# Kernel tuning notes

Hardware: AMD Instinct MI355X
Metric: run time of the kernel (lower is better)

The kernel has to match this reference:

```python
import jax, jax.numpy as jnp
import numpy as np

B, T, C, H = 4, 4096, 256, 64

def setup_inputs() -> dict:
    key = jax.random.key(0)
    k1, k2, k3, k4 = jax.random.split(key, 4)
    x = jax.random.normal(k1, (B, T, C), dtype=jnp.float32)
    # DenseSynapse weights ~ uniform(-0.1, 0.1); randn spec approximated faithfully in math, init dist irrelevant to correctness
    Wk = jax.random.uniform(k2, (C, H), minval=-0.1, maxval=0.1, dtype=jnp.float32)
    Wq = jax.random.uniform(k3, (C, H), minval=-0.1, maxval=0.1, dtype=jnp.float32)
    Wv = jax.random.uniform(k4, (C, H), minval=-0.1, maxval=0.1, dtype=jnp.float32)
    return {"x": x, "Wk": Wk, "Wq": Wq, "Wv": Wv}

def reference(x, Wk, Wq, Wv):
    Bq, Tq, Cq = x.shape
    # linear projections (DenseSynapse.advance_state with Rscale=1, no bias): x @ W
    k = jnp.einsum('btc,ch->bth', x, Wk)
    q = jnp.einsum('btc,ch->bth', x, Wq)
    v = jnp.einsum('btc,ch->bth', x, Wv)
    # scores scaled by C**-0.5 (n_embd, as in source)
    wei = jnp.einsum('bqh,bkh->bqk', q, k) * (Cq ** -0.5)
    mask = jnp.tril(jnp.ones((Tq, Tq), dtype=bool))
    wei = jnp.where(mask, wei, -jnp.inf)
    wei = jax.nn.softmax(wei, axis=-1)
    # dropout deterministic (eval) in reference
    out = jnp.einsum('bqk,bkh->bqh', wei, v)
    return out
```

## Files before the change

kernel.cpp:

```cpp
#include <hip/hip_runtime.h>
#include <hip/hip_bf16.h>
#include <math.h>

#define Bb   4
#define T    4096
#define Cc   256
#define Hh   64
#define BT   (Bb*T)
#define CHUNK 8
#define CPB  288

using f32x4  = __attribute__((ext_vector_type(4))) float;
using short8 = __attribute__((ext_vector_type(8))) short;

__device__ __forceinline__ ushort f2bf(float f) {
    unsigned u = __builtin_bit_cast(unsigned, f);
    return (ushort)((u + 0x8000u) >> 16);
}
__device__ __forceinline__ float bf2f(ushort u) {
    return __builtin_bit_cast(float, (unsigned)u << 16);
}
__device__ __forceinline__ int swzb(int row, int cb) { return (row<<7) + (cb ^ ((row&7)<<4)); }
__device__ __forceinline__ int swzx(int row, int cb) { return (row<<9) + (cb ^ ((row&7)<<4)); }
__device__ __forceinline__ int chunk_prefix(int qt) {
    const int a = qt >> 3, r = qt & 7;
    return 4*a*(a+1) + r*(a+1);
}

#define GLOAD16(g, l) __builtin_amdgcn_global_load_lds( \
    (const __attribute__((address_space(1))) unsigned*)(g), \
    (__attribute__((address_space(3))) unsigned*)(l), 16, 0, 0)

__global__ __launch_bounds__(256) void wtrans(
    const float* __restrict__ Wq, const float* __restrict__ Wk,
    const float* __restrict__ Wv, ushort* __restrict__ WtG)
{
    __shared__ float wl[256][65];
    const int t = threadIdx.x;
    const int m = blockIdx.x;
    const float* W = (m==0) ? Wq : (m==1) ? Wk : Wv;
    const float scale = (m==0) ? 0.0625f : 1.0f;
    for (int idx = t; idx < 4096; idx += 256) {
        const float4 v4 = ((const float4*)W)[idx];
        const int c = idx >> 4;
        const int h = (idx & 15) * 4;
        wl[c][h+0]=v4.x*scale; wl[c][h+1]=v4.y*scale;
        wl[c][h+2]=v4.z*scale; wl[c][h+3]=v4.w*scale;
    }
    __syncthreads();
    const int h  = t & 63;
    const int n  = m*64 + h;
    const int c0 = (t >> 6) * 64;
    for (int c = c0; c < c0 + 64; c += 4) {
        ushort4 o;
        o.x=f2bf(wl[c+0][h]); o.y=f2bf(wl[c+1][h]);
        o.z=f2bf(wl[c+2][h]); o.w=f2bf(wl[c+3][h]);
        *(ushort4*)((char*)WtG + n*512 + ((c*2) ^ ((n&7)<<4))) = o;
    }
}

__global__ __launch_bounds__(256) void proj_mfma(
    const float* __restrict__ x, const ushort* __restrict__ WtG,
    ushort* __restrict__ qo, ushort* __restrict__ ko, ushort* __restrict__ vtG)
{
    __shared__ ushort xls[64*256];
    __shared__ ushort wls[192*256];
    const int t = threadIdx.x, w = t>>6, lane = t&63, g = lane>>4, ln = lane&15;
    const int blk = blockIdx.x;
    const long rowbase = (long)blk * 64;
    const int b    = blk >> 6;
    const int trow = (blk & 63) * 64;

    {
        const char* src = (const char*)WtG + (long)lane*16;
        for (int c = w; c < 96; c += 4)
            GLOAD16(src + c*1024, (char*)wls + c*1024);
    }
    for (int j = 0; j < 16; ++j) {
        const int idx = t + j*256;
        const int row = idx >> 6;
        const int c4  = (idx & 63) * 4;
        const float4 xv = ((const float4*)x)[(rowbase + row)*64 + (c4>>2)];
        ushort4 o; o.x=f2bf(xv.x); o.y=f2bf(xv.y); o.z=f2bf(xv.z); o.w=f2bf(xv.w);
        *(ushort4*)((char*)xls + swzx(row, c4*2)) = o;
    }
    __syncthreads();

    short8 xf[8];
    #pragma unroll
    for (int ks = 0; ks < 8; ++ks)
        xf[ks] = *(const short8*)((const char*)xls + swzx(w*16+ln, ks*64 + g*16));

    #pragma unroll
    for (int nt = 0; nt < 12; ++nt) {
        f32x4 acc = (f32x4){0.f,0.f,0.f,0.f};
        #pragma unroll
        for (int ks = 0; ks < 8; ++ks) {
            const short8 wf = *(const short8*)((const char*)wls + swzx(nt*16+ln, ks*64 + g*16));
            acc = (nt < 8) ? __builtin_amdgcn_mfma_f32_16x16x32_bf16(wf, xf[ks], acc, 0,0,0)
                           : __builtin_amdgcn_mfma_f32_16x16x32_bf16(xf[ks], wf, acc, 0,0,0);
        }
        ushort4 o; o.x=f2bf(acc[0]); o.y=f2bf(acc[1]); o.z=f2bf(acc[2]); o.w=f2bf(acc[3]);
        if (nt < 4) {
            *(ushort4*)(qo + (rowbase + w*16 + ln)*64 + nt*16 + g*4) = o;
        } else if (nt < 8) {
            *(ushort4*)(ko + (rowbase + w*16 + ln)*64 + (nt-4)*16 + g*4) = o;
        } else {
            *(ushort4*)(vtG + ((long)b*64 + (nt-8)*16 + ln)*T + trow + w*16 + g*4) = o;
        }
    }
}

__global__ __launch_bounds__(256) void attn_mfma(
    const ushort* __restrict__ q, const ushort* __restrict__ k,
    const ushort* __restrict__ vt,
    ushort* __restrict__ part_o, float* __restrict__ part_ml)
{
    __shared__ ushort kls[2][64*64];
    __shared__ ushort vtls[2][64*64];
    __shared__ ushort pls[4][16*64];

    const int bid   = blockIdx.x;
    const int b     = bid & 3;
    const int w2    = (CPB - 1) - (bid >> 2);
    int qt = 0, c = 0;
    {
        int acc = 0;
        for (int qq = 0; qq < 64; ++qq) {
            const int n = (qq >> 3) + 1;
            if (w2 < acc + n) { qt = qq; c = w2 - acc; break; }
            acc += n;
        }
    }
    const int kt0   = c * CHUNK;
    const int ntile = min(qt, kt0 + CHUNK - 1) - kt0 + 1;
    const int pid   = b*CPB + chunk_prefix(qt) + c;

    const int t = threadIdx.x, w = t>>6, lane = t&63, g = lane>>4, ln = lane&15;
    const int lrow = lane >> 3;
    const int lc16 = ((lane & 7) ^ lrow) * 16;
    const char* kbase = (const char*)k  + ((long)b*T)*128;
    const char* vbase = (const char*)vt + ((long)b*64)*(long)T*2;

    #define STAGE(bufi, ktile) do { \
        _Pragma("unroll") for (int j = 0; j < 2; ++j) { const int ci = w*2 + j; \
            GLOAD16(kbase + (long)(ktile)*8192 + ci*1024 + lrow*128 + lc16, \
                    (char*)kls[bufi] + ci*1024); \
            GLOAD16(vbase + ((long)(8*ci + lrow))*8192 + (long)(ktile)*128 + lc16, \
                    (char*)vtls[bufi] + ci*1024); \
        } } while(0)

    short8 qf[2];
    {
        const ushort* qp = q + ((long)(b*T + qt*64 + w*16 + ln))*64;
        qf[0] = *(const short8*)(qp + g*8);
        qf[1] = *(const short8*)(qp + 32 + g*8);
    }
    f32x4 oacc[4];
    #pragma unroll
    for (int i = 0; i < 4; ++i) oacc[i] = (f32x4){0.f,0.f,0.f,0.f};
    float mrun[4], lpart[4];
    #pragma unroll
    for (int r = 0; r < 4; ++r) { mrun[r] = -INFINITY; lpart[r] = 0.f; }

    STAGE(0, kt0);
    for (int it = 0; it < ntile; ++it) {
        const int kt  = kt0 + it;
        const int cur = it & 1;
        __syncthreads();
        if (it + 1 < ntile) STAGE(cur^1, kt + 1);

        f32x4 sf[4];
        #pragma unroll
        for (int i = 0; i < 4; ++i) sf[i] = (f32x4){0.f,0.f,0.f,0.f};
        __builtin_amdgcn_s_setprio(1);
        #pragma unroll
        for (int ks = 0; ks < 2; ++ks)
            #pragma unroll
            for (int nt = 0; nt < 4; ++nt) {
                const short8 bk = *(const short8*)((const char*)kls[cur] +
                                     swzb(nt*16 + ln, ks*64 + g*16));
                sf[nt] = __builtin_amdgcn_mfma_f32_16x16x32_bf16(qf[ks], bk, sf[nt], 0,0,0);
            }
        __builtin_amdgcn_s_setprio(0);
        if (kt == qt) {
            #pragma unroll
            for (int nt = 0; nt < 4; ++nt)
                #pragma unroll
                for (int r = 0; r < 4; ++r)
                    if (nt*16 + ln > w*16 + g*4 + r) sf[nt][r] = -INFINITY;
        }

        bool ok = true;
        #pragma unroll
        for (int nt = 0; nt < 4; ++nt)
            #pragma unroll
            for (int r = 0; r < 4; ++r)
                ok &= (sf[nt][r] <= mrun[r] + 8.f);
        if (!__all(ok)) {
            float mt[4];
            #pragma unroll
            for (int r = 0; r < 4; ++r)
                mt[r] = fmaxf(fmaxf(sf[0][r], sf[1][r]), fmaxf(sf[2][r], sf[3][r]));
            #pragma unroll
            for (int d = 1; d < 16; d <<= 1)
                #pragma unroll
                for (int r = 0; r < 4; ++r)
                    mt[r] = fmaxf(mt[r], __shfl_xor(mt[r], d));
            #pragma unroll
            for (int r = 0; r < 4; ++r) {
                const float mn = fmaxf(mrun[r], mt[r]);
                const float corr = __expf(mrun[r] - mn);
                mrun[r] = mn;
                lpart[r] *= corr;
                #pragma unroll
                for (int nt = 0; nt < 4; ++nt) oacc[nt][r] *= corr;
            }
        }

        #pragma unroll
        for (int nt = 0; nt < 4; ++nt)
            #pragma unroll
            for (int r = 0; r < 4; ++r) {
                const float p = __expf(sf[nt][r] - mrun[r]);
                lpart[r] += p;
                *(ushort*)((char*)pls[w] + swzb(g*4 + r, (nt*16 + ln)*2)) = f2bf(p);
            }

        __builtin_amdgcn_s_setprio(1);
        #pragma unroll
        for (int ks = 0; ks < 2; ++ks) {
            const short8 pa = *(const short8*)((const char*)pls[w] +
                                 swzb(ln, ks*64 + g*16));
            #pragma unroll
            for (int nt = 0; nt < 4; ++nt) {
                const short8 bv = *(const short8*)((const char*)vtls[cur] +
                                     swzb(nt*16 + ln, ks*64 + g*16));
                oacc[nt] = __builtin_amdgcn_mfma_f32_16x16x32_bf16(pa, bv, oacc[nt], 0,0,0);
            }
        }
        __builtin_amdgcn_s_setprio(0);
    }
    #undef STAGE

    #pragma unroll
    for (int d = 1; d < 16; d <<= 1)
        #pragma unroll
        for (int r = 0; r < 4; ++r)
            lpart[r] += __shfl_xor(lpart[r], d);

    const long pbase = (long)pid * 4096;
    #pragma unroll
    for (int nt = 0; nt < 4; ++nt)
        #pragma unroll
        for (int r = 0; r < 4; ++r)
            part_o[pbase + (w*16 + g*4 + r)*64 + nt*16 + ln] = f2bf(oacc[nt][r]);
    if (ln == 0)
        #pragma unroll
        for (int r = 0; r < 4; ++r) {
            part_ml[(long)pid*128 + (w*16 + g*4 + r)*2 + 0] = mrun[r];
            part_ml[(long)pid*128 + (w*16 + g*4 + r)*2 + 1] = lpart[r];
        }
}

__global__ __launch_bounds__(256) void attn_merge(
    const ushort* __restrict__ part_o, const float* __restrict__ part_ml,
    float* __restrict__ out)
{
    const int bid = blockIdx.x;
    const int b = bid >> 6, qt = bid & 63;
    const int t = threadIdx.x, row = t >> 2, sub = t & 3;
    const int nseg = (qt >> 3) + 1;
    const int base = b*CPB + chunk_prefix(qt);

    float ms[CHUNK], ls[CHUNK];
    float mstar = -INFINITY;
    for (int s = 0; s < nseg; ++s) {
        ms[s] = part_ml[(long)(base+s)*128 + row*2 + 0];
        ls[s] = part_ml[(long)(base+s)*128 + row*2 + 1];
        mstar = fmaxf(mstar, ms[s]);
    }
    float acc[16];
    #pragma unroll
    for (int i = 0; i < 16; ++i) acc[i] = 0.f;
    float lsum = 0.f;
    for (int s = 0; s < nseg; ++s) {
        const float wgt = __expf(ms[s] - mstar);
        lsum += ls[s] * wgt;
        const short8* po = (const short8*)(part_o + (long)(base+s)*4096 + row*64 + sub*16);
        #pragma unroll
        for (int j = 0; j < 2; ++j) {
            const short8 v8 = po[j];
            #pragma unroll
            for (int e = 0; e < 8; ++e)
                acc[j*8+e] += wgt * bf2f((ushort)v8[e]);
        }
    }
    const float inv = 1.f / lsum;
    float* op = out + ((long)b*T + qt*64 + row)*64 + sub*16;
    #pragma unroll
    for (int j = 0; j < 4; ++j)
        ((float4*)op)[j] = make_float4(acc[4*j+0]*inv, acc[4*j+1]*inv,
                                       acc[4*j+2]*inv, acc[4*j+3]*inv);
}

extern "C" void kernel_launch(void* const* d_in, const int* in_sizes, int n_in,
                              void* d_out, int out_size, void* d_ws, size_t ws_size,
                              hipStream_t stream)
{
    const float* x  = (const float*)d_in[0];
    const float* Wk = (const float*)d_in[1];
    const float* Wq = (const float*)d_in[2];
    const float* Wv = (const float*)d_in[3];

    char* w8 = (char*)d_ws;
    ushort* qb      = (ushort*)(w8);
    ushort* kb      = (ushort*)(w8 + (2l<<20));
    ushort* vt      = (ushort*)(w8 + (4l<<20));
    ushort* Wt      = (ushort*)(w8 + (6l<<20));
    ushort* part_o  = (ushort*)(w8 + (7l<<20));
    float*  part_ml = (float*) (w8 + (17l<<20));

    wtrans    <<<3,         256, 0, stream>>>(Wq, Wk, Wv, Wt);
    proj_mfma <<<BT/64,     256, 0, stream>>>(x, Wt, qb, kb, vt);
    attn_mfma <<<Bb*CPB,    256, 0, stream>>>(qb, kb, vt, part_o, part_ml);
    attn_merge<<<Bb*(T/64), 256, 0, stream>>>(part_o, part_ml, (float*)d_out);
}
```

Before: 55.65 us.

## Switch attention to 32x32 MFMA with 128-row query tiles and register P

Rewrites the attention kernel to use 32x32x16 bf16 MFMAs computing S^T, with each block covering 128 query rows (32 per wave) instead of 64, which halves the number of split-KV chunks and partials. The P matrix is now built in registers through lane shuffles, so the per-wave LDS staging of P is gone. Softmax uses exp2 with log2(e) folded into the Q scale, and the rescale threshold is widened. The merge kernel is reworked to match the new transposed partial layout with one thread per row, which gives it fewer blocks and more registers per thread.

```diff
diff --git a/kernel.cpp b/kernel.cpp
--- a/kernel.cpp
+++ b/kernel.cpp
@@ -7,12 +7,16 @@
 #define Cc   256
 #define Hh   64
 #define BT   (Bb*T)
-#define CHUNK 8
-#define CPB  288
+#define CPB  144
 
 using f32x4  = __attribute__((ext_vector_type(4))) float;
+using f32x16 = __attribute__((ext_vector_type(16))) float;
 using short8 = __attribute__((ext_vector_type(8))) short;
-
+using int4v  = __attribute__((ext_vector_type(4))) int;
+
+__device__ __forceinline__ float fexp2(float x) {
+    return __builtin_amdgcn_exp2f(x);
+}
 __device__ __forceinline__ ushort f2bf(float f) {
     unsigned u = __builtin_bit_cast(unsigned, f);
     return (ushort)((u + 0x8000u) >> 16);
@@ -23,8 +27,8 @@
 __device__ __forceinline__ int swzb(int row, int cb) { return (row<<7) + (cb ^ ((row&7)<<4)); }
 __device__ __forceinline__ int swzx(int row, int cb) { return (row<<9) + (cb ^ ((row&7)<<4)); }
 __device__ __forceinline__ int chunk_prefix(int qt) {
-    const int a = qt >> 3, r = qt & 7;
-    return 4*a*(a+1) + r*(a+1);
+    const int a = qt >> 2, r = qt & 3;
+    return 2*a*(a+1) + r*(a+1);
 }
 
 #define GLOAD16(g, l) __builtin_amdgcn_global_load_lds( \
@@ -39,7 +43,7 @@
     const int t = threadIdx.x;
     const int m = blockIdx.x;
     const float* W = (m==0) ? Wq : (m==1) ? Wk : Wv;
-    const float scale = (m==0) ? 0.0625f : 1.0f;
+    const float scale = (m==0) ? 0.09016844005556021f : 1.0f;
     for (int idx = t; idx < 4096; idx += 256) {
         const float4 v4 = ((const float4*)W)[idx];
         const int c = idx >> 4;
@@ -116,27 +120,28 @@
     const ushort* __restrict__ vt,
     ushort* __restrict__ part_o, float* __restrict__ part_ml)
 {
-    __shared__ ushort kls[2][64*64];
-    __shared__ ushort vtls[2][64*64];
-    __shared__ ushort pls[4][16*64];
-
-    const int bid   = blockIdx.x;
-    const int b     = bid & 3;
-    const int w2    = (CPB - 1) - (bid >> 2);
+    __shared__ ushort kls[2][4096];
+    __shared__ ushort vtls[2][4096];
+
+    const int bid = blockIdx.x;
+    const int b   = bid & 3;
+    const int w2  = (CPB - 1) - (bid >> 2);
     int qt = 0, c = 0;
     {
         int acc = 0;
-        for (int qq = 0; qq < 64; ++qq) {
-            const int n = (qq >> 3) + 1;
+        for (int qq = 0; qq < 32; ++qq) {
+            const int n = (qq + 4) >> 2;
             if (w2 < acc + n) { qt = qq; c = w2 - acc; break; }
             acc += n;
         }
     }
-    const int kt0   = c * CHUNK;
-    const int ntile = min(qt, kt0 + CHUNK - 1) - kt0 + 1;
+    const int kt0   = c * 8;
+    const int ktend = min(2*qt + 1, kt0 + 7);
+    const int ntile = ktend - kt0 + 1;
     const int pid   = b*CPB + chunk_prefix(qt) + c;
 
-    const int t = threadIdx.x, w = t>>6, lane = t&63, g = lane>>4, ln = lane&15;
+    const int t = threadIdx.x, w = t>>6, lane = t&63;
+    const int l5 = lane & 31, g5 = lane >> 5;
     const int lrow = lane >> 3;
     const int lc16 = ((lane & 7) ^ lrow) * 16;
     const char* kbase = (const char*)k  + ((long)b*T)*128;
@@ -150,18 +155,20 @@
                     (char*)vtls[bufi] + ci*1024); \
         } } while(0)
 
-    short8 qf[2];
+    const int qmin = qt*128 + w*32;
+    const int qrow = qmin + l5;
+    short8 qf[4];
     {
-        const ushort* qp = q + ((long)(b*T + qt*64 + w*16 + ln))*64;
-        qf[0] = *(const short8*)(qp + g*8);
-        qf[1] = *(const short8*)(qp + 32 + g*8);
-    }
-    f32x4 oacc[4];
-    #pragma unroll
-    for (int i = 0; i < 4; ++i) oacc[i] = (f32x4){0.f,0.f,0.f,0.f};
-    float mrun[4], lpart[4];
-    #pragma unroll
-    for (int r = 0; r < 4; ++r) { mrun[r] = -INFINITY; lpart[r] = 0.f; }
+        const ushort* qp = q + ((long)(b*T + qrow))*64;
+        #pragma unroll
+        for (int hs = 0; hs < 4; ++hs)
+            qf[hs] = *(const short8*)(qp + hs*16 + g5*8);
+    }
+
+    f32x16 o0, o1;
+    #pragma unroll
+    for (int i = 0; i < 16; ++i) { o0[i] = 0.f; o1[i] = 0.f; }
+    float mrun = -INFINITY, lpart = 0.f;
 
     STAGE(0, kt0);
     for (int it = 0; it < ntile; ++it) {
@@ -169,139 +176,144 @@
         const int cur = it & 1;
         __syncthreads();
         if (it + 1 < ntile) STAGE(cur^1, kt + 1);
-
-        f32x4 sf[4];
-        #pragma unroll
-        for (int i = 0; i < 4; ++i) sf[i] = (f32x4){0.f,0.f,0.f,0.f};
+        if (kt*64 > qmin + 31) continue;
+
+        f32x16 s0, s1;
+        #pragma unroll
+        for (int i = 0; i < 16; ++i) { s0[i] = 0.f; s1[i] = 0.f; }
         __builtin_amdgcn_s_setprio(1);
         #pragma unroll
-        for (int ks = 0; ks < 2; ++ks)
+        for (int hs = 0; hs < 4; ++hs) {
+            const short8 kf0 = *(const short8*)((const char*)kls[cur] + swzb(l5,    hs*32 + g5*16));
+            s0 = __builtin_amdgcn_mfma_f32_32x32x16_bf16(kf0, qf[hs], s0, 0, 0, 0);
+            const short8 kf1 = *(const short8*)((const char*)kls[cur] + swzb(32+l5, hs*32 + g5*16));
+            s1 = __builtin_amdgcn_mfma_f32_32x32x16_bf16(kf1, qf[hs], s1, 0, 0, 0);
+        }
+        __builtin_amdgcn_s_setprio(0);
+
+        if (kt*64 + 63 > qmin) {
             #pragma unroll
-            for (int nt = 0; nt < 4; ++nt) {
-                const short8 bk = *(const short8*)((const char*)kls[cur] +
-                                     swzb(nt*16 + ln, ks*64 + g*16));
-                sf[nt] = __builtin_amdgcn_mfma_f32_16x16x32_bf16(qf[ks], bk, sf[nt], 0,0,0);
+            for (int reg = 0; reg < 16; ++reg) {
+                const int kl = (reg&3) + 8*(reg>>2) + 4*g5;
+                if (kt*64 + kl      > qrow) s0[reg] = -INFINITY;
+                if (kt*64 + 32 + kl > qrow) s1[reg] = -INFINITY;
             }
+        }
+
+        bool ok = true;
+        #pragma unroll
+        for (int r = 0; r < 16; ++r) {
+            ok &= (s0[r] <= mrun + 11.5f);
+            ok &= (s1[r] <= mrun + 11.5f);
+        }
+        if (!__all(ok)) {
+            float mt = s0[0];
+            #pragma unroll
+            for (int r = 1; r < 16; ++r) mt = fmaxf(mt, s0[r]);
+            #pragma unroll
+            for (int r = 0; r < 16; ++r) mt = fmaxf(mt, s1[r]);
+            mt = fmaxf(mt, __shfl_xor(mt, 32));
+            const float mn = fmaxf(mrun, mt);
+            const float corr = fexp2(mrun - mn);
+            lpart *= corr;
+            #pragma unroll
+            for (int r = 0; r < 16; ++r) { o0[r] *= corr; o1[r] *= corr; }
+            mrun = mn;
+        }
+
+        unsigned u0[8], u1[8];
+        #pragma unroll
+        for (int i = 0; i < 8; ++i) {
+            const float pa = fexp2(s0[2*i+0] - mrun);
+            const float pb = fexp2(s0[2*i+1] - mrun);
+            lpart += pa + pb;
+            u0[i] = (unsigned)f2bf(pa) | ((unsigned)f2bf(pb) << 16);
+            const float pc = fexp2(s1[2*i+0] - mrun);
+            const float pd = fexp2(s1[2*i+1] - mrun);
+            lpart += pc + pd;
+            u1[i] = (unsigned)f2bf(pc) | ((unsigned)f2bf(pd) << 16);
+        }
+        unsigned x0[8], x1[8];
+        #pragma unroll
+        for (int i = 0; i < 8; ++i) {
+            x0[i] = (unsigned)__shfl_xor((int)u0[i], 32);
+            x1[i] = (unsigned)__shfl_xor((int)u1[i], 32);
+        }
+        int4v pw[4];
+        #pragma unroll
+        for (int s = 0; s < 2; ++s) {
+            pw[s].x   = g5 ? (int)x0[4*s+2] : (int)u0[4*s+0];
+            pw[s].y   = g5 ? (int)x0[4*s+3] : (int)u0[4*s+1];
+            pw[s].z   = g5 ? (int)u0[4*s+2] : (int)x0[4*s+0];
+            pw[s].w   = g5 ? (int)u0[4*s+3] : (int)x0[4*s+1];
+            pw[2+s].x = g5 ? (int)x1[4*s+2] : (int)u1[4*s+0];
+            pw[2+s].y = g5 ? (int)x1[4*s+3] : (int)u1[4*s+1];
+            pw[2+s].z = g5 ? (int)u1[4*s+2] : (int)x1[4*s+0];
+            pw[2+s].w = g5 ? (int)u1[4*s+3] : (int)x1[4*s+1];
+        }
+
+        __builtin_amdgcn_s_setprio(1);
+        #pragma unroll
+        for (int ks2 = 0; ks2 < 4; ++ks2) {
+            const short8 pa = __builtin_bit_cast(short8, pw[ks2]);
+            const short8 vf0 = *(const short8*)((const char*)vtls[cur] + swzb(l5,    ks2*32 + g5*16));
+            o0 = __builtin_amdgcn_mfma_f32_32x32x16_bf16(vf0, pa, o0, 0, 0, 0);
+            const short8 vf1 = *(const short8*)((const char*)vtls[cur] + swzb(32+l5, ks2*32 + g5*16));
+            o1 = __builtin_amdgcn_mfma_f32_32x32x16_bf16(vf1, pa, o1, 0, 0, 0);
+        }
         __builtin_amdgcn_s_setprio(0);
-        if (kt == qt) {
-            #pragma unroll
-            for (int nt = 0; nt < 4; ++nt)
-                #pragma unroll
-                for (int r = 0; r < 4; ++r)
-                    if (nt*16 + ln > w*16 + g*4 + r) sf[nt][r] = -INFINITY;
-        }
-
-        bool ok = true;
-        #pragma unroll
-        for (int nt = 0; nt < 4; ++nt)
-            #pragma unroll
-            for (int r = 0; r < 4; ++r)
-                ok &= (sf[nt][r] <= mrun[r] + 8.f);
-        if (!__all(ok)) {
-            float mt[4];
-            #pragma unroll
-            for (int r = 0; r < 4; ++r)
-                mt[r] = fmaxf(fmaxf(sf[0][r], sf[1][r]), fmaxf(sf[2][r], sf[3][r]));
-            #pragma unroll
-            for (int d = 1; d < 16; d <<= 1)
-                #pragma unroll
-                for (int r = 0; r < 4; ++r)
-                    mt[r] = fmaxf(mt[r], __shfl_xor(mt[r], d));
-            #pragma unroll
-            for (int r = 0; r < 4; ++r) {
-                const float mn = fmaxf(mrun[r], mt[r]);
-                const float corr = __expf(mrun[r] - mn);
-                mrun[r] = mn;
-                lpart[r] *= corr;
-                #pragma unroll
-                for (int nt = 0; nt < 4; ++nt) oacc[nt][r] *= corr;
-            }
-        }
-
-        #pragma unroll
-        for (int nt = 0; nt < 4; ++nt)
-            #pragma unroll
-            for (int r = 0; r < 4; ++r) {
-                const float p = __expf(sf[nt][r] - mrun[r]);
-                lpart[r] += p;
-                *(ushort*)((char*)pls[w] + swzb(g*4 + r, (nt*16 + ln)*2)) = f2bf(p);
-            }
-
-        __builtin_amdgcn_s_setprio(1);
-        #pragma unroll
-        for (int ks = 0; ks < 2; ++ks) {
-            const short8 pa = *(const short8*)((const char*)pls[w] +
-                                 swzb(ln, ks*64 + g*16));
-            #pragma unroll
-            for (int nt = 0; nt < 4; ++nt) {
-                const short8 bv = *(const short8*)((const char*)vtls[cur] +
-                                     swzb(nt*16 + ln, ks*64 + g*16));
-                oacc[nt] = __builtin_amdgcn_mfma_f32_16x16x32_bf16(pa, bv, oacc[nt], 0,0,0);
-            }
-        }
-        __builtin_amdgcn_s_setprio(0);
     }
     #undef STAGE
 
-    #pragma unroll
-    for (int d = 1; d < 16; d <<= 1)
-        #pragma unroll
-        for (int r = 0; r < 4; ++r)
-            lpart[r] += __shfl_xor(lpart[r], d);
-
-    const long pbase = (long)pid * 4096;
-    #pragma unroll
-    for (int nt = 0; nt < 4; ++nt)
-        #pragma unroll
-        for (int r = 0; r < 4; ++r)
-            part_o[pbase + (w*16 + g*4 + r)*64 + nt*16 + ln] = f2bf(oacc[nt][r]);
-    if (ln == 0)
-        #pragma unroll
-        for (int r = 0; r < 4; ++r) {
-            part_ml[(long)pid*128 + (w*16 + g*4 + r)*2 + 0] = mrun[r];
-            part_ml[(long)pid*128 + (w*16 + g*4 + r)*2 + 1] = lpart[r];
-        }
-}
-
-__global__ __launch_bounds__(256) void attn_merge(
+    const float ltot = lpart + __shfl_xor(lpart, 32);
+    if (g5 == 0) {
+        part_ml[((long)pid*128 + w*32 + l5)*2 + 0] = mrun;
+        part_ml[((long)pid*128 + w*32 + l5)*2 + 1] = ltot;
+    }
+    ushort* po = part_o + (long)pid*8192;
+    #pragma unroll
+    for (int reg = 0; reg < 16; ++reg) {
+        const int h = (reg&3) + 8*(reg>>2) + 4*g5;
+        po[(h     )*128 + w*32 + l5] = f2bf(o0[reg]);
+        po[(h + 32)*128 + w*32 + l5] = f2bf(o1[reg]);
+    }
+}
+
+__global__ __launch_bounds__(128) void attn_merge(
     const ushort* __restrict__ part_o, const float* __restrict__ part_ml,
     float* __restrict__ out)
 {
     const int bid = blockIdx.x;
-    const int b = bid >> 6, qt = bid & 63;
-    const int t = threadIdx.x, row = t >> 2, sub = t & 3;
-    const int nseg = (qt >> 3) + 1;
+    const int b = bid >> 5, qt = bid & 31;
+    const int t = threadIdx.x;
+    const int nseg = (qt + 4) >> 2;
     const int base = b*CPB + chunk_prefix(qt);
 
-    float ms[CHUNK], ls[CHUNK];
+    float ms[8], ls[8];
     float mstar = -INFINITY;
     for (int s = 0; s < nseg; ++s) {
-        ms[s] = part_ml[(long)(base+s)*128 + row*2 + 0];
-        ls[s] = part_ml[(long)(base+s)*128 + row*2 + 1];
+        ms[s] = part_ml[((long)(base+s)*128 + t)*2 + 0];
+        ls[s] = part_ml[((long)(base+s)*128 + t)*2 + 1];
         mstar = fmaxf(mstar, ms[s]);
     }
-    float acc[16];
-    #pragma unroll
-    for (int i = 0; i < 16; ++i) acc[i] = 0.f;
+    float acc[64];
+    #pragma unroll
+    for (int h = 0; h < 64; ++h) acc[h] = 0.f;
     float lsum = 0.f;
     for (int s = 0; s < nseg; ++s) {
-        const float wgt = __expf(ms[s] - mstar);
+        const float wgt = fexp2(ms[s] - mstar);
         lsum += ls[s] * wgt;
-        const short8* po = (const short8*)(part_o + (long)(base+s)*4096 + row*64 + sub*16);
-        #pragma unroll
-        for (int j = 0; j < 2; ++j) {
-            const short8 v8 = po[j];
-            #pragma unroll
-            for (int e = 0; e < 8; ++e)
-                acc[j*8+e] += wgt * bf2f((ushort)v8[e]);
-        }
+        const ushort* po = part_o + (long)(base+s)*8192 + t;
+        #pragma unroll
+        for (int h = 0; h < 64; ++h)
+            acc[h] += wgt * bf2f(po[h*128]);
     }
     const float inv = 1.f / lsum;
-    float* op = out + ((long)b*T + qt*64 + row)*64 + sub*16;
-    #pragma unroll
-    for (int j = 0; j < 4; ++j)
-        ((float4*)op)[j] = make_float4(acc[4*j+0]*inv, acc[4*j+1]*inv,
-                                       acc[4*j+2]*inv, acc[4*j+3]*inv);
+    float* op = out + ((long)b*T + qt*128 + t)*64;
+    #pragma unroll
+    for (int h4 = 0; h4 < 16; ++h4)
+        ((float4*)op)[h4] = make_float4(acc[4*h4+0]*inv, acc[4*h4+1]*inv,
+                                        acc[4*h4+2]*inv, acc[4*h4+3]*inv);
 }
 
 extern "C" void kernel_launch(void* const* d_in, const int* in_sizes, int n_in,
@@ -321,8 +333,8 @@
     ushort* part_o  = (ushort*)(w8 + (7l<<20));
     float*  part_ml = (float*) (w8 + (17l<<20));
 
-    wtrans    <<<3,         256, 0, stream>>>(Wq, Wk, Wv, Wt);
-    proj_mfma <<<BT/64,     256, 0, stream>>>(x, Wt, qb, kb, vt);
-    attn_mfma <<<Bb*CPB,    256, 0, stream>>>(qb, kb, vt, part_o, part_ml);
-    attn_merge<<<Bb*(T/64), 256, 0, stream>>>(part_o, part_ml, (float*)d_out);
-}
+    wtrans    <<<3,       256, 0, stream>>>(Wq, Wk, Wv, Wt);
+    proj_mfma <<<BT/64,   256, 0, stream>>>(x, Wt, qb, kb, vt);
+    attn_mfma <<<Bb*CPB,  256, 0, stream>>>(qb, kb, vt, part_o, part_ml);
+    attn_merge<<<Bb*32,   128, 0, stream>>>(part_o, part_ml, (float*)d_out);
+}
```

After: 115.7 us. 108% more time.
